# Performance work log

Measured on AMD Instinct MI355X. Metric: run time of the kernel, lower is better.

## Reference

```python
import jax, jax.numpy as jnp
import numpy as np

MARGIN = 0.2  # cfg.SOLVER.PROTO_MARGIN
EPS = 1e-8    # torch cosine_similarity default eps

B, K, D = 1024, 127, 512


def setup_inputs() -> dict:
    key = jax.random.key(0)
    k1, k2, k3 = jax.random.split(key, 3)
    ref = jax.random.normal(k1, (B, D), dtype=jnp.float32)
    pos = jax.random.normal(k2, (B, D), dtype=jnp.float32)
    neg = jax.random.normal(k3, (B, K, D), dtype=jnp.float32)
    return {"ref": ref, "pos": pos, "neg": neg}


def _safe_norm(x, axis):
    # torch cosine_similarity clamps each norm to at least eps
    return jnp.maximum(jnp.linalg.norm(x, axis=axis), EPS)


def reference(ref, pos, neg):
    # ref, pos: [B, D]; neg: [B, K, D]
    ref_n = ref / _safe_norm(ref, axis=1)[:, None]            # [B, D]
    pos_n = pos / _safe_norm(pos, axis=1)[:, None]            # [B, D]
    neg_n = neg / _safe_norm(neg, axis=2)[:, :, None]         # [B, K, D]

    pos_sim = jnp.einsum("bd,bd->b", ref_n, pos_n)           # [B]
    neg_sim = jnp.einsum("bd,bkd->bk", ref_n, neg_n)         # [B, K]

    # per-sample triplet loss: mean over K of max(0, m + neg_sim - pos_sim)
    per_sample = jnp.mean(jnp.maximum(MARGIN + neg_sim - pos_sim[:, None], 0.0), axis=1)  # [B]
    return jnp.mean(per_sample)  # average over batch
```

## Files before the change

kernel.cpp:

```cpp
#include <hip/hip_runtime.h>


#define NB 1024
#define NK 127
#define ND 512
#define MARGIN 0.2f
#define CEPS 1e-8f

__device__ __forceinline__ float dot4(const float4 a, const float4 b) {
    return a.x * b.x + a.y * b.y + a.z * b.z + a.w * b.w;
}

__global__ __launch_bounds__(256) void triplet_main(
    const float* __restrict__ ref, const float* __restrict__ pos,
    const float* __restrict__ neg, float* __restrict__ partial)
{
    const int b    = blockIdx.x;
    const int tid  = threadIdx.x;
    const int wave = tid >> 6;
    const int lane = tid & 63;
    const int sub  = lane >> 4;
    const int sl   = lane & 15;

    const float* refr = ref + (size_t)b * ND;
    const float* posr = pos + (size_t)b * ND;

    float4 r[8];
    #pragma unroll
    for (int j = 0; j < 8; ++j) r[j] = *(const float4*)(refr + sl * 4 + j * 64);

    float rs = 0.0f, ps = 0.0f, pd = 0.0f;
    #pragma unroll
    for (int j = 0; j < 8; ++j) {
        const float4 p = *(const float4*)(posr + sl * 4 + j * 64);
        rs += dot4(r[j], r[j]);
        ps += dot4(p, p);
        pd += dot4(r[j], p);
    }
    #pragma unroll
    for (int off = 1; off <= 8; off <<= 1) {
        rs += __shfl_xor(rs, off);
        ps += __shfl_xor(ps, off);
        pd += __shfl_xor(pd, off);
    }

    const float inv_r   = 1.0f / fmaxf(sqrtf(rs), CEPS);
    const float pos_sim = pd * inv_r * (1.0f / fmaxf(sqrtf(ps), CEPS));

    float acc = 0.0f;
    const float* negb = neg + (size_t)b * (NK * ND);

    for (int g = wave; g < 32; g += 4) {
        const int  k     = 4 * g + sub;
        const bool valid = (k < NK);
        const int  kk    = valid ? k : (NK - 1);
        const float* nr  = negb + (size_t)kk * ND + sl * 4;

        float4 n[8];
        #pragma unroll
        for (int j = 0; j < 8; ++j) n[j] = *(const float4*)(nr + j * 64);

        float nd = 0.0f, ns = 0.0f;
        #pragma unroll
        for (int j = 0; j < 8; ++j) {
            nd += dot4(r[j], n[j]);
            ns += dot4(n[j], n[j]);
        }
        #pragma unroll
        for (int off = 1; off <= 8; off <<= 1) {
            nd += __shfl_xor(nd, off);
            ns += __shfl_xor(ns, off);
        }
        const float sim = nd * inv_r * (1.0f / fmaxf(sqrtf(ns), CEPS));
        acc += valid ? fmaxf(MARGIN + sim - pos_sim, 0.0f) : 0.0f;
    }

    acc += __shfl_xor(acc, 16);
    acc += __shfl_xor(acc, 32);

    __shared__ float sacc[4];
    if (lane == 0) sacc[wave] = acc;
    __syncthreads();
    if (tid == 0) partial[b] = (sacc[0] + sacc[1]) + (sacc[2] + sacc[3]);
}

__global__ __launch_bounds__(256) void triplet_reduce(
    const float* __restrict__ partial, float* __restrict__ out)
{
    float s = 0.0f;
    for (int i = threadIdx.x; i < NB; i += 256) s += partial[i];
    #pragma unroll
    for (int off = 32; off; off >>= 1) s += __shfl_xor(s, off);
    __shared__ float w[4];
    if ((threadIdx.x & 63) == 0) w[threadIdx.x >> 6] = s;
    __syncthreads();
    if (threadIdx.x == 0)
        out[0] = ((w[0] + w[1]) + (w[2] + w[3])) * (1.0f / ((float)NB * (float)NK));
}

extern "C" void kernel_launch(void* const* d_in, const int* in_sizes, int n_in,
                              void* d_out, int out_size, void* d_ws, size_t ws_size,
                              hipStream_t stream) {
    const float* ref = (const float*)d_in[0];
    const float* pos = (const float*)d_in[1];
    const float* neg = (const float*)d_in[2];
    float* out     = (float*)d_out;
    float* partial = (float*)d_ws;

    triplet_main<<<NB, 256, 0, stream>>>(ref, pos, neg, partial);
    triplet_reduce<<<1, 256, 0, stream>>>(partial, out);
}
```

Measured before the change: 49.82 us.

## Fuse final reduction via last-block atomic counter and double-buffer nontemporal neg loads

```diff
diff --git a/kernel.cpp b/kernel.cpp
--- a/kernel.cpp
+++ b/kernel.cpp
@@ -7,13 +7,41 @@
 #define MARGIN 0.2f
 #define CEPS 1e-8f
 
-__device__ __forceinline__ float dot4(const float4 a, const float4 b) {
+typedef float floatx4 __attribute__((ext_vector_type(4)));
+
+__device__ __forceinline__ float dot4(const floatx4 a, const floatx4 b) {
     return a.x * b.x + a.y * b.y + a.z * b.z + a.w * b.w;
 }
 
-__global__ __launch_bounds__(256) void triplet_main(
+__device__ __forceinline__ void load8nt(floatx4 (&n)[8], const float* __restrict__ p) {
+    #pragma unroll
+    for (int j = 0; j < 8; ++j)
+        n[j] = __builtin_nontemporal_load((const floatx4*)(p + j * 64));
+}
+
+__device__ __forceinline__ void reduce_group(
+    const floatx4 (&r)[8], const floatx4 (&n)[8], bool valid,
+    float inv_r, float pos_sim, float& acc)
+{
+    float nd = 0.0f, ns = 0.0f;
+    #pragma unroll
+    for (int j = 0; j < 8; ++j) {
+        nd += dot4(r[j], n[j]);
+        ns += dot4(n[j], n[j]);
+    }
+    #pragma unroll
+    for (int off = 1; off <= 8; off <<= 1) {
+        nd += __shfl_xor(nd, off);
+        ns += __shfl_xor(ns, off);
+    }
+    const float sim = nd * inv_r * (1.0f / fmaxf(sqrtf(ns), CEPS));
+    acc += valid ? fmaxf(MARGIN + sim - pos_sim, 0.0f) : 0.0f;
+}
+
+__global__ __launch_bounds__(256, 4) void triplet_fused(
     const float* __restrict__ ref, const float* __restrict__ pos,
-    const float* __restrict__ neg, float* __restrict__ partial)
+    const float* __restrict__ neg, float* __restrict__ partial,
+    unsigned* __restrict__ counter, float* __restrict__ out)
 {
     const int b    = blockIdx.x;
     const int tid  = threadIdx.x;
@@ -25,14 +53,14 @@
     const float* refr = ref + (size_t)b * ND;
     const float* posr = pos + (size_t)b * ND;
 
-    float4 r[8];
+    floatx4 r[8];
     #pragma unroll
-    for (int j = 0; j < 8; ++j) r[j] = *(const float4*)(refr + sl * 4 + j * 64);
+    for (int j = 0; j < 8; ++j) r[j] = *(const floatx4*)(refr + sl * 4 + j * 64);
 
     float rs = 0.0f, ps = 0.0f, pd = 0.0f;
     #pragma unroll
     for (int j = 0; j < 8; ++j) {
-        const float4 p = *(const float4*)(posr + sl * 4 + j * 64);
+        const floatx4 p = *(const floatx4*)(posr + sl * 4 + j * 64);
         rs += dot4(r[j], r[j]);
         ps += dot4(p, p);
         pd += dot4(r[j], p);
@@ -43,36 +71,31 @@
         ps += __shfl_xor(ps, off);
         pd += __shfl_xor(pd, off);
     }
-
     const float inv_r   = 1.0f / fmaxf(sqrtf(rs), CEPS);
     const float pos_sim = pd * inv_r * (1.0f / fmaxf(sqrtf(ps), CEPS));
 
-    float acc = 0.0f;
     const float* negb = neg + (size_t)b * (NK * ND);
 
-    for (int g = wave; g < 32; g += 4) {
-        const int  k     = 4 * g + sub;
-        const bool valid = (k < NK);
-        const int  kk    = valid ? k : (NK - 1);
-        const float* nr  = negb + (size_t)kk * ND + sl * 4;
+    float acc = 0.0f;
+    floatx4 bufA[8], bufB[8];
 
-        float4 n[8];
-        #pragma unroll
-        for (int j = 0; j < 8; ++j) n[j] = *(const float4*)(nr + j * 64);
+    auto gaddr = [&](int it) -> const float* {
+        const int k  = 4 * (wave + 4 * it) + sub;
+        const int kk = (k < NK) ? k : (NK - 1);
+        return negb + (size_t)kk * ND + sl * 4;
+    };
+    auto gvalid = [&](int it) -> bool {
+        return 4 * (wave + 4 * it) + sub < NK;
+    };
 
-        float nd = 0.0f, ns = 0.0f;
-        #pragma unroll
-        for (int j = 0; j < 8; ++j) {
-            nd += dot4(r[j], n[j]);
-            ns += dot4(n[j], n[j]);
-        }
-        #pragma unroll
-        for (int off = 1; off <= 8; off <<= 1) {
-            nd += __shfl_xor(nd, off);
-            ns += __shfl_xor(ns, off);
-        }
-        const float sim = nd * inv_r * (1.0f / fmaxf(sqrtf(ns), CEPS));
-        acc += valid ? fmaxf(MARGIN + sim - pos_sim, 0.0f) : 0.0f;
+    load8nt(bufA, gaddr(0));
+    #pragma unroll
+    for (int p2 = 0; p2 < 4; ++p2) {
+        const int it = 2 * p2;
+        load8nt(bufB, gaddr(it + 1));
+        reduce_group(r, bufA, gvalid(it), inv_r, pos_sim, acc);
+        if (p2 < 3) load8nt(bufA, gaddr(it + 2));
+        reduce_group(r, bufB, gvalid(it + 1), inv_r, pos_sim, acc);
     }
 
     acc += __shfl_xor(acc, 16);
@@ -81,21 +104,32 @@
     __shared__ float sacc[4];
     if (lane == 0) sacc[wave] = acc;
     __syncthreads();
-    if (tid == 0) partial[b] = (sacc[0] + sacc[1]) + (sacc[2] + sacc[3]);
-}
 
-__global__ __launch_bounds__(256) void triplet_reduce(
-    const float* __restrict__ partial, float* __restrict__ out)
-{
-    float s = 0.0f;
-    for (int i = threadIdx.x; i < NB; i += 256) s += partial[i];
-    #pragma unroll
-    for (int off = 32; off; off >>= 1) s += __shfl_xor(s, off);
-    __shared__ float w[4];
-    if ((threadIdx.x & 63) == 0) w[threadIdx.x >> 6] = s;
+    __shared__ bool amLast;
+    if (tid == 0) {
+        const float total = (sacc[0] + sacc[1]) + (sacc[2] + sacc[3]);
+        __hip_atomic_store(&partial[b], total, __ATOMIC_RELEASE,
+                           __HIP_MEMORY_SCOPE_AGENT);
+        const unsigned t = __hip_atomic_fetch_add(counter, 1u, __ATOMIC_ACQ_REL,
+                                                  __HIP_MEMORY_SCOPE_AGENT);
+        amLast = (t == NB - 1);
+    }
     __syncthreads();
-    if (threadIdx.x == 0)
-        out[0] = ((w[0] + w[1]) + (w[2] + w[3])) * (1.0f / ((float)NB * (float)NK));
+
+    if (amLast) {
+        __threadfence();
+        float s = 0.0f;
+        for (int i = tid; i < NB; i += 256)
+            s += __hip_atomic_load(&partial[i], __ATOMIC_RELAXED,
+                                   __HIP_MEMORY_SCOPE_AGENT);
+        #pragma unroll
+        for (int off = 32; off; off >>= 1) s += __shfl_xor(s, off);
+        __shared__ float w[4];
+        if (lane == 0) w[wave] = s;
+        __syncthreads();
+        if (tid == 0)
+            out[0] = ((w[0] + w[1]) + (w[2] + w[3])) * (1.0f / ((float)NB * (float)NK));
+    }
 }
 
 extern "C" void kernel_launch(void* const* d_in, const int* in_sizes, int n_in,
@@ -104,9 +138,11 @@
     const float* ref = (const float*)d_in[0];
     const float* pos = (const float*)d_in[1];
     const float* neg = (const float*)d_in[2];
-    float* out     = (float*)d_out;
-    float* partial = (float*)d_ws;
+    float* out = (float*)d_out;
 
-    triplet_main<<<NB, 256, 0, stream>>>(ref, pos, neg, partial);
-    triplet_reduce<<<1, 256, 0, stream>>>(partial, out);
+    unsigned* counter = (unsigned*)d_ws;
+    float*    partial = (float*)((char*)d_ws + 256);
+
+    (void)hipMemsetAsync(counter, 0, sizeof(unsigned), stream);
+    triplet_fused<<<NB, 256, 0, stream>>>(ref, pos, neg, partial, counter, out);
 }
```

Measured after the change: 143.0 us. 2.87x slower.
